# Performance work log

Hardware: AMD Instinct MI355X
Metric: run time of the kernel (lower is better)

The kernel has to match this reference:

```python
import jax, jax.numpy as jnp
import numpy as np

IN_FEATURES = 4096
OUT_FEATURES = 4096
BLOCKSIZE = 64
FP4_CODEBOOK = np.array([0.0, 0.0052, 0.6667, 1.0, 0.3333, 0.5, 0.1667, 0.25,
                         0.0, -0.0052, -0.6667, -1.0, -0.3333, -0.5, -0.1667, -0.25],
                        dtype=np.float32)


def setup_inputs() -> dict:
    key = jax.random.key(0)
    k1, k2, k3, k4 = jax.random.split(key, 4)
    n_elements = OUT_FEATURES * IN_FEATURES
    n_blocks = n_elements // BLOCKSIZE
    x = jax.random.normal(k1, (4, 2048, IN_FEATURES), dtype=jnp.float32)
    weight_packed = jax.random.randint(k2, (n_elements // 2,), 0, 256, dtype=jnp.int32)
    scale = jax.random.uniform(k3, (n_blocks,), dtype=jnp.float32)
    bias = jax.random.normal(k4, (OUT_FEATURES,), dtype=jnp.float32)
    return {"x": x, "weight_packed": weight_packed, "scale": scale, "bias": bias}


def reference(x, weight_packed, scale, bias):
    codebook = jnp.asarray(FP4_CODEBOOK, dtype=x.dtype)
    # Unpack two 4-bit indices per byte: high nibble first, then low nibble.
    high = (weight_packed >> 4) & 15
    low = weight_packed & 15
    indices = jnp.stack([high, low], axis=1).reshape(-1)  # [n_elements]
    # LUT dequant + per-block scale broadcast.
    deq = codebook[indices].reshape(-1, BLOCKSIZE) * scale[:, None]  # [n_blocks, blocksize]
    weight = deq.reshape(OUT_FEATURES, IN_FEATURES)
    # F.linear(x, W, b) = x @ W.T + b
    return jnp.einsum('bsi,oi->bso', x, weight) + bias
```

## Files before the change

kernel.cpp:

```cpp
#include <hip/hip_runtime.h>
#include <stdint.h>
#include <stddef.h>

#define IN_F 4096
#define OUT_F 4096
#define M_TOT 8192

#define BM 128
#define BN 128
#define BK 64

#define BM2 256
#define BN2 256
#define BK2 64
#define NT2 (IN_F / BK2)

typedef __attribute__((ext_vector_type(8))) short short8;
typedef __attribute__((ext_vector_type(4))) float f32x4;
typedef __attribute__((ext_vector_type(4))) float float4v;
typedef __attribute__((ext_vector_type(4))) unsigned short u16x4;
typedef __attribute__((ext_vector_type(8))) unsigned short u16x8;
typedef unsigned short u16;

__constant__ float c_lut[16] = {
  0.0f, 0.0052f, 0.6667f, 1.0f, 0.3333f, 0.5f, 0.1667f, 0.25f,
  0.0f, -0.0052f, -0.6667f, -1.0f, -0.3333f, -0.5f, -0.1667f, -0.25f
};

__device__ __forceinline__ u16 f2bf(float f) {
  unsigned int x = __float_as_uint(f);
  x += 0x7fffu + ((x >> 16) & 1u);
  return (u16)(x >> 16);
}

__device__ __forceinline__ void gload_lds16(const u16* g, u16* lds) {
  __builtin_amdgcn_global_load_lds(
      (const __attribute__((address_space(1))) unsigned int*)g,
      (__attribute__((address_space(3))) unsigned int*)lds, 16, 0, 0);
}

#define BARRIER() do { asm volatile("" ::: "memory"); \
                       __builtin_amdgcn_s_barrier();  \
                       asm volatile("" ::: "memory"); } while (0)
#define LGW(n) do { asm volatile("s_waitcnt lgkmcnt(" #n ")" ::: "memory"); \
                    __builtin_amdgcn_sched_barrier(0); } while (0)
#define VMW(n) asm volatile("s_waitcnt vmcnt(" #n ")" ::: "memory")

__global__ __launch_bounds__(256) void k_prep(const float* __restrict__ x,
                                              u16* __restrict__ a,
                                              const int* __restrict__ wp,
                                              const float* __restrict__ scale,
                                              u16* __restrict__ b) {
  if (blockIdx.x < 512) {
    __shared__ float lut[16];
    if (threadIdx.x < 16) lut[threadIdx.x] = c_lut[threadIdx.x];
    __syncthreads();
    const int ng = (OUT_F * IN_F / 2) / 4;
    const int stride = 512 * 256;
    for (int t = blockIdx.x * 256 + threadIdx.x; t < ng; t += stride) {
      int4 p = ((const int4*)wp)[t];
      float s = scale[t >> 3];
      int by[4] = {p.x, p.y, p.z, p.w};
      u16x8 o;
#pragma unroll
      for (int q = 0; q < 4; ++q) {
        o[2 * q]     = f2bf(lut[(by[q] >> 4) & 15] * s);
        o[2 * q + 1] = f2bf(lut[by[q] & 15] * s);
      }
      ((u16x8*)b)[t] = o;
    }
  } else {
    const int n8 = (M_TOT * IN_F) / 8;
    const int stride = 4096 * 256;
    for (int t = (blockIdx.x - 512) * 256 + threadIdx.x; t < n8; t += stride) {
      float4v f0 = ((const float4v*)x)[2 * t];
      float4v f1 = ((const float4v*)x)[2 * t + 1];
      u16x8 o;
      o[0] = f2bf(f0.x); o[1] = f2bf(f0.y); o[2] = f2bf(f0.z); o[3] = f2bf(f0.w);
      o[4] = f2bf(f1.x); o[5] = f2bf(f1.y); o[6] = f2bf(f1.z); o[7] = f2bf(f1.w);
      ((u16x8*)a)[t] = o;
    }
  }
}


__device__ __forceinline__ void st_b(const u16* __restrict__ B, u16* dst,
                                     int nBase, int kt, int h, int k,
                                     int wave, int srow, int scol) {
  const int r0 = 64 * (wave >> 1) + 32 * h + 16 * k + 8 * (wave & 1);
  gload_lds16(B + (size_t)(nBase + r0 + srow) * IN_F + kt + scol, dst + r0 * BK2);
}
__device__ __forceinline__ void st_a(const u16* __restrict__ A, u16* dst,
                                     int mBase, int kt, int h, int k,
                                     int wave, int srow, int scol) {
  const int r0 = 128 * (wave >> 2) + 64 * h + 32 * k + 8 * (wave & 3);
  gload_lds16(A + (size_t)(mBase + r0 + srow) * IN_F + kt + scol, dst + r0 * BK2);
}

__device__ __forceinline__ void rd_b(short8 d[2][2], const u16* Bs_c, int bBase,
                                     int co0, int co1, int h) {
#pragma unroll
  for (int jj = 0; jj < 2; ++jj) {
    const int ro = bBase + (h * 2 + jj) * (16 * BK2);
    d[jj][0] = *(const short8*)&Bs_c[ro + co0];
    d[jj][1] = *(const short8*)&Bs_c[ro + co1];
  }
}
__device__ __forceinline__ void rd_a(short8 d[4][2], const u16* As_c, int aBase,
                                     int co0, int co1, int h) {
#pragma unroll
  for (int ii = 0; ii < 4; ++ii) {
    const int ro = aBase + (h * 4 + ii) * (16 * BK2);
    d[ii][0] = *(const short8*)&As_c[ro + co0];
    d[ii][1] = *(const short8*)&As_c[ro + co1];
  }
}
__device__ __forceinline__ void mma8(f32x4 acc[8][4], const short8 a[4][2],
                                     const short8 b[2][2], int i0, int j0) {
#pragma unroll
  for (int k2 = 0; k2 < 2; ++k2)
#pragma unroll
    for (int ii = 0; ii < 4; ++ii)
#pragma unroll
      for (int jj = 0; jj < 2; ++jj)
        acc[i0 + ii][j0 + jj] = __builtin_amdgcn_mfma_f32_16x16x32_bf16(
            a[ii][k2], b[jj][k2], acc[i0 + ii][j0 + jj], 0, 0, 0);
}

__global__ __launch_bounds__(512, 2) void k_gemm256(const u16* __restrict__ A,
                                                    const u16* __restrict__ B,
                                                    const float* __restrict__ bias,
                                                    float* __restrict__ C) {
  __shared__ u16 As[2][BM2 * BK2];
  __shared__ u16 Bs[2][BN2 * BK2];

  const int tid  = threadIdx.x;
  const int lane = tid & 63;
  const int wave = tid >> 6;

  const int bid   = blockIdx.x;
  const int xcd   = bid & 7;
  const int kk    = bid >> 3;
  const int tileM = (xcd >> 1) * 8 + (kk >> 3);
  const int tileN = (xcd & 1) * 8 + (kk & 7);
  const int mBase = tileM * BM2;
  const int nBase = tileN * BN2;

  const int wm = (wave >> 2) * 128;
  const int wn = (wave & 3) * 64;

  const int srow = lane >> 3;
  const int scol = ((lane & 7) ^ srow) * 8;

  const int frow = lane & 15;
  const int fx   = frow & 7;
  const int cq   = lane >> 4;
  const int co0  = ((cq ^ fx) << 3);
  const int co1  = (((4 + cq) ^ fx) << 3);
  const int aBase = (wm + frow) * BK2;
  const int bBase = (wn + frow) * BK2;

  f32x4 acc[8][4] = {};
  short8 aC[4][2], aN[4][2], b0[2][2], b1[2][2];

  st_b(B, Bs[0], nBase, 0, 0, 0, wave, srow, scol);
  st_b(B, Bs[0], nBase, 0, 0, 1, wave, srow, scol);
  st_b(B, Bs[0], nBase, 0, 1, 0, wave, srow, scol);
  st_b(B, Bs[0], nBase, 0, 1, 1, wave, srow, scol);
  st_a(A, As[0], mBase, 0, 0, 0, wave, srow, scol);
  st_a(A, As[0], mBase, 0, 0, 1, wave, srow, scol);
  st_a(A, As[0], mBase, 0, 1, 0, wave, srow, scol);
  st_a(A, As[0], mBase, 0, 1, 1, wave, srow, scol);
  st_b(B, Bs[1], nBase, BK2, 0, 0, wave, srow, scol);
  st_b(B, Bs[1], nBase, BK2, 0, 1, wave, srow, scol);
  st_a(A, As[1], mBase, BK2, 0, 0, wave, srow, scol);
  st_a(A, As[1], mBase, BK2, 0, 1, wave, srow, scol);
  st_b(B, Bs[1], nBase, BK2, 1, 0, wave, srow, scol);
  st_b(B, Bs[1], nBase, BK2, 1, 1, wave, srow, scol);
  VMW(6);
  BARRIER();
  rd_a(aC, As[0], aBase, co0, co1, 0);

  for (int t = 0; t < NT2; ++t) {
    const int c = t & 1;
    u16* AsC = As[c];
    u16* BsC = Bs[c];
    u16* AsO = As[c ^ 1];

    if (t < NT2 - 1) { VMW(6); } else { VMW(0); }
    rd_b(b0, BsC, bBase, co0, co1, 0);
    __builtin_amdgcn_sched_barrier(0);
    rd_b(b1, BsC, bBase, co0, co1, 1);
    if (t + 1 < NT2) st_a(A, AsO, mBase, (t + 1) * BK2, 1, 0, wave, srow, scol);
    BARRIER();
    LGW(4);
    __builtin_amdgcn_s_setprio(1);
    mma8(acc, aC, b0, 0, 0);
    __builtin_amdgcn_s_setprio(0);

    rd_a(aN, AsC, aBase, co0, co1, 1);
    if (t + 1 < NT2) st_a(A, AsO, mBase, (t + 1) * BK2, 1, 1, wave, srow, scol);
    BARRIER();
    LGW(8);
    __builtin_amdgcn_s_setprio(1);
    mma8(acc, aC, b1, 0, 2);
    __builtin_amdgcn_s_setprio(0);

    VMW(2);
    if (t + 2 < NT2) {
      st_b(B, BsC, nBase, (t + 2) * BK2, 0, 0, wave, srow, scol);
      st_b(B, BsC, nBase, (t + 2) * BK2, 0, 1, wave, srow, scol);
      st_a(A, AsC, mBase, (t + 2) * BK2, 0, 0, wave, srow, scol);
    }
    BARRIER();
    LGW(0);
    __builtin_amdgcn_s_setprio(1);
    mma8(acc, aN, b1, 4, 2);
    __builtin_amdgcn_s_setprio(0);

    if (t + 1 < NT2) rd_a(aC, AsO, aBase, co0, co1, 0);
    if (t + 2 < NT2) {
      st_a(A, AsC, mBase, (t + 2) * BK2, 0, 1, wave, srow, scol);
      st_b(B, BsC, nBase, (t + 2) * BK2, 1, 0, wave, srow, scol);
      st_b(B, BsC, nBase, (t + 2) * BK2, 1, 1, wave, srow, scol);
    }
    BARRIER();
    __builtin_amdgcn_s_setprio(1);
    mma8(acc, aN, b0, 4, 0);
    __builtin_amdgcn_s_setprio(0);
  }

  const int ccol = lane & 15;
  const int crow = (lane >> 4) * 4;
#pragma unroll
  for (int j = 0; j < 4; ++j) {
    const int col = nBase + wn + j * 16 + ccol;
    const float bv = bias[col];
#pragma unroll
    for (int i = 0; i < 8; ++i) {
      const size_t rb = (size_t)(mBase + wm + i * 16 + crow) * OUT_F + col;
#pragma unroll
      for (int tt = 0; tt < 4; ++tt)
        C[rb + (size_t)tt * OUT_F] = acc[i][j][tt] + bv;
    }
  }
}

__global__ __launch_bounds__(256) void k_gemm_fused(const float* __restrict__ X,
                                                    const int* __restrict__ WP,
                                                    const float* __restrict__ scale,
                                                    const float* __restrict__ bias,
                                                    float* __restrict__ C) {
  __shared__ u16 As[BM * BK];
  __shared__ u16 Bs[BN * BK];
  __shared__ float lut[16];
  const int tid = threadIdx.x;
  if (tid < 16) lut[tid] = c_lut[tid];
  const int lane = tid & 63;
  const int wave = tid >> 6;
  const int mBase = blockIdx.y * BM;
  const int nBase = blockIdx.x * BN;
  const int wm = (wave >> 1) * 64;
  const int wn = (wave & 1) * 64;
  const int frow = lane & 15;
  const int fx   = lane & 7;
  const int cq   = lane >> 4;
  f32x4 acc[4][4] = {};
  __syncthreads();

  for (int kt = 0; kt < IN_F; kt += BK) {
#pragma unroll
    for (int i = 0; i < 8; ++i) {
      const int g = tid + i * 256;
      const int r = g >> 4, c = (g & 15) * 4;
      float4v f = *(const float4v*)&X[(size_t)(mBase + r) * IN_F + kt + c];
      u16x4 o;
      o.x = f2bf(f.x); o.y = f2bf(f.y); o.z = f2bf(f.z); o.w = f2bf(f.w);
      *(u16x4*)&As[r * BK + ((((c >> 3) ^ (r & 7)) << 3) | (c & 7))] = o;
    }
#pragma unroll
    for (int i = 0; i < 4; ++i) {
      const int g = tid + i * 256;
      const int r = g >> 3, c4 = (g & 7) * 4;
      int4 p = *(const int4*)&WP[(size_t)(nBase + r) * (IN_F / 2) + (kt >> 1) + c4];
      const float s = scale[(nBase + r) * 64 + (kt >> 6)];
      int by[4] = {p.x, p.y, p.z, p.w};
      u16x8 o;
#pragma unroll
      for (int q = 0; q < 4; ++q) {
        o[2 * q]     = f2bf(lut[(by[q] >> 4) & 15] * s);
        o[2 * q + 1] = f2bf(lut[by[q] & 15] * s);
      }
      *(u16x8*)&Bs[r * BK + (((g & 7) ^ (r & 7)) << 3)] = o;
    }
    __syncthreads();
#pragma unroll
    for (int ks = 0; ks < BK; ks += 32) {
      const int co = (((ks >> 3) + cq) ^ fx) << 3;
      short8 a[4], b[4];
#pragma unroll
      for (int i = 0; i < 4; ++i)
        a[i] = *(const short8*)&As[(wm + i * 16 + frow) * BK + co];
#pragma unroll
      for (int j = 0; j < 4; ++j)
        b[j] = *(const short8*)&Bs[(wn + j * 16 + frow) * BK + co];
#pragma unroll
      for (int i = 0; i < 4; ++i)
#pragma unroll
        for (int j = 0; j < 4; ++j)
          acc[i][j] = __builtin_amdgcn_mfma_f32_16x16x32_bf16(a[i], b[j], acc[i][j], 0, 0, 0);
    }
    __syncthreads();
  }

  const int ccol = lane & 15;
  const int crow = (lane >> 4) * 4;
#pragma unroll
  for (int j = 0; j < 4; ++j) {
    const int col = nBase + wn + j * 16 + ccol;
    const float bv = bias[col];
#pragma unroll
    for (int i = 0; i < 4; ++i) {
      const size_t rb = (size_t)(mBase + wm + i * 16 + crow) * OUT_F + col;
#pragma unroll
      for (int t = 0; t < 4; ++t)
        C[rb + (size_t)t * OUT_F] = acc[i][j][t] + bv;
    }
  }
}

extern "C" void kernel_launch(void* const* d_in, const int* in_sizes, int n_in,
                              void* d_out, int out_size, void* d_ws, size_t ws_size,
                              hipStream_t stream) {
  const float* x  = (const float*)d_in[0];
  const int*   wp = (const int*)d_in[1];
  const float* sc = (const float*)d_in[2];
  const float* bi = (const float*)d_in[3];
  float* out = (float*)d_out;

  const size_t bBytes = (size_t)OUT_F * IN_F * 2;
  const size_t aBytes = (size_t)M_TOT * IN_F * 2;

  if (ws_size >= aBytes + bBytes) {
    u16* B = (u16*)d_ws;
    u16* A = (u16*)((char*)d_ws + bBytes);
    k_prep<<<4608, 256, 0, stream>>>(x, A, wp, sc, B);
    k_gemm256<<<(M_TOT / BM2) * (OUT_F / BN2), 512, 0, stream>>>(A, B, bi, out);
  } else {
    dim3 grid(OUT_F / BN, M_TOT / BM);
    k_gemm_fused<<<grid, 256, 0, stream>>>(x, wp, sc, bi, out);
  }
}
```

Before: 483.7 us.

## Reschedule GEMM main loop to prefetch B one tile ahead and reorder MMA quarters

Restructures the software pipeline of the 256x256 bf16 GEMM main loop. B tiles are now loaded only one K-step ahead into the other buffer, while A keeps a partial two-step lookahead. The MMA quarters are reordered so the next aC and b0 fragments are read from LDS before the final MMA of the iteration. vmcnt waits and barriers are rebalanced into four evenly split phases. The aim is to overlap global loads, LDS reads and MFMA work more evenly, at the cost of a shorter prefetch distance for B, which could expose memory latency.

```diff
diff --git a/kernel.cpp b/kernel.cpp
--- a/kernel.cpp
+++ b/kernel.cpp
@@ -163,35 +163,36 @@
   f32x4 acc[8][4] = {};
   short8 aC[4][2], aN[4][2], b0[2][2], b1[2][2];
 
+  st_a(A, As[0], mBase, 0, 0, 0, wave, srow, scol);
+  st_a(A, As[0], mBase, 0, 0, 1, wave, srow, scol);
   st_b(B, Bs[0], nBase, 0, 0, 0, wave, srow, scol);
   st_b(B, Bs[0], nBase, 0, 0, 1, wave, srow, scol);
   st_b(B, Bs[0], nBase, 0, 1, 0, wave, srow, scol);
   st_b(B, Bs[0], nBase, 0, 1, 1, wave, srow, scol);
-  st_a(A, As[0], mBase, 0, 0, 0, wave, srow, scol);
-  st_a(A, As[0], mBase, 0, 0, 1, wave, srow, scol);
   st_a(A, As[0], mBase, 0, 1, 0, wave, srow, scol);
   st_a(A, As[0], mBase, 0, 1, 1, wave, srow, scol);
-  st_b(B, Bs[1], nBase, BK2, 0, 0, wave, srow, scol);
-  st_b(B, Bs[1], nBase, BK2, 0, 1, wave, srow, scol);
   st_a(A, As[1], mBase, BK2, 0, 0, wave, srow, scol);
   st_a(A, As[1], mBase, BK2, 0, 1, wave, srow, scol);
-  st_b(B, Bs[1], nBase, BK2, 1, 0, wave, srow, scol);
-  st_b(B, Bs[1], nBase, BK2, 1, 1, wave, srow, scol);
-  VMW(6);
+  VMW(2);
   BARRIER();
   rd_a(aC, As[0], aBase, co0, co1, 0);
+  rd_b(b0, Bs[0], bBase, co0, co1, 0);
 
   for (int t = 0; t < NT2; ++t) {
     const int c = t & 1;
     u16* AsC = As[c];
     u16* BsC = Bs[c];
     u16* AsO = As[c ^ 1];
-
-    if (t < NT2 - 1) { VMW(6); } else { VMW(0); }
-    rd_b(b0, BsC, bBase, co0, co1, 0);
-    __builtin_amdgcn_sched_barrier(0);
+    u16* BsO = Bs[c ^ 1];
+    const int kt1 = (t + 1) * BK2;
+    const int kt2 = (t + 2) * BK2;
+
     rd_b(b1, BsC, bBase, co0, co1, 1);
-    if (t + 1 < NT2) st_a(A, AsO, mBase, (t + 1) * BK2, 1, 0, wave, srow, scol);
+    if (t + 1 < NT2) {
+      st_b(B, BsO, nBase, kt1, 0, 0, wave, srow, scol);
+      st_b(B, BsO, nBase, kt1, 0, 1, wave, srow, scol);
+    }
+    if (t < NT2 - 3) { VMW(4); } else { VMW(0); }
     BARRIER();
     LGW(4);
     __builtin_amdgcn_s_setprio(1);
@@ -199,34 +200,39 @@
     __builtin_amdgcn_s_setprio(0);
 
     rd_a(aN, AsC, aBase, co0, co1, 1);
-    if (t + 1 < NT2) st_a(A, AsO, mBase, (t + 1) * BK2, 1, 1, wave, srow, scol);
+    if (t + 1 < NT2) {
+      st_b(B, BsO, nBase, kt1, 1, 0, wave, srow, scol);
+      st_b(B, BsO, nBase, kt1, 1, 1, wave, srow, scol);
+    }
+    if (t < NT2 - 3) { VMW(4); } else { VMW(0); }
     BARRIER();
     LGW(8);
     __builtin_amdgcn_s_setprio(1);
     mma8(acc, aC, b1, 0, 2);
     __builtin_amdgcn_s_setprio(0);
 
-    VMW(2);
+    if (t + 1 < NT2) rd_a(aC, AsO, aBase, co0, co1, 0);
+    if (t + 1 < NT2) {
+      st_a(A, AsO, mBase, kt1, 1, 0, wave, srow, scol);
+      st_a(A, AsO, mBase, kt1, 1, 1, wave, srow, scol);
+    }
+    if (t < NT2 - 3) { VMW(4); } else { VMW(0); }
+    BARRIER();
+    if (t + 1 < NT2) { LGW(8); } else { LGW(0); }
+    __builtin_amdgcn_s_setprio(1);
+    mma8(acc, aN, b0, 4, 0);
+    __builtin_amdgcn_s_setprio(0);
+
+    if (t + 1 < NT2) rd_b(b0, BsO, bBase, co0, co1, 0);
     if (t + 2 < NT2) {
-      st_b(B, BsC, nBase, (t + 2) * BK2, 0, 0, wave, srow, scol);
-      st_b(B, BsC, nBase, (t + 2) * BK2, 0, 1, wave, srow, scol);
-      st_a(A, AsC, mBase, (t + 2) * BK2, 0, 0, wave, srow, scol);
-    }
+      st_a(A, AsC, mBase, kt2, 0, 0, wave, srow, scol);
+      st_a(A, AsC, mBase, kt2, 0, 1, wave, srow, scol);
+    }
+    if (t < NT2 - 3) { VMW(4); } else { VMW(0); }
     BARRIER();
-    LGW(0);
+    __builtin_amdgcn_sched_barrier(0);
     __builtin_amdgcn_s_setprio(1);
     mma8(acc, aN, b1, 4, 2);
-    __builtin_amdgcn_s_setprio(0);
-
-    if (t + 1 < NT2) rd_a(aC, AsO, aBase, co0, co1, 0);
-    if (t + 2 < NT2) {
-      st_a(A, AsC, mBase, (t + 2) * BK2, 0, 1, wave, srow, scol);
-      st_b(B, BsC, nBase, (t + 2) * BK2, 1, 0, wave, srow, scol);
-      st_b(B, BsC, nBase, (t + 2) * BK2, 1, 1, wave, srow, scol);
-    }
-    BARRIER();
-    __builtin_amdgcn_s_setprio(1);
-    mma8(acc, aN, b0, 4, 0);
     __builtin_amdgcn_s_setprio(0);
   }
 
```

Measured after the change: 518.0 us. +7.1%, slower.
